# Kernel optimization log

Measured on AMD Instinct MI355X. Metric: run time of the kernel, lower is better.

## Reference

```python
import jax, jax.numpy as jnp
import numpy as np

NUM_STUDENTS = 50000
NUM_KP = 100
KD = 128          # knowledge_dim
HID = 256         # hidden_dim
B = 16384
K = 20            # max_knowledge_points


def setup_inputs() -> dict:
    key = jax.random.key(0)
    ks = jax.random.split(key, 16)
    inp = {
        "student_indices": jax.random.randint(ks[0], (B,), 0, NUM_STUDENTS, dtype=jnp.int32),
        "kp_indices": jax.random.randint(ks[1], (B, K), 0, NUM_KP, dtype=jnp.int32),
        "kp_lengths": jax.random.randint(ks[2], (B,), 0, K + 1, dtype=jnp.int32),
        # learned parameters
        "emb": jax.random.normal(ks[3], (NUM_STUDENTS, NUM_KP, KD), dtype=jnp.float32),
        # attention: Linear(KD,HID) -> tanh -> Linear(HID,1) -> softmax(dim=1)
        "W1": jax.random.normal(ks[4], (KD, HID), dtype=jnp.float32) * 0.05,
        "b1": jnp.zeros((HID,), jnp.float32),
        "w2": jax.random.normal(ks[5], (HID, 1), dtype=jnp.float32) * 0.05,
        "b2": jnp.zeros((1,), jnp.float32),
        # MLP: Linear(KD,HID)-ReLU-Linear(HID,HID//2)-ReLU-Linear(HID//2,1)-Sigmoid
        "M1": jax.random.normal(ks[6], (KD, HID), dtype=jnp.float32) * 0.05,
        "mb1": jnp.zeros((HID,), jnp.float32),
        "M2": jax.random.normal(ks[7], (HID, HID // 2), dtype=jnp.float32) * 0.05,
        "mb2": jnp.zeros((HID // 2,), jnp.float32),
        "M3": jax.random.normal(ks[8], (HID // 2, 1), dtype=jnp.float32) * 0.05,
        "mb3": jnp.zeros((1,), jnp.float32),
    }
    return inp


def reference(student_indices, kp_indices, kp_lengths, emb, W1, b1, w2, b2,
              M1, mb1, M2, mb2, M3, mb3):
    # ragged gather -> padded [B, K, KD]; padded slots are zero (as in the torch loop)
    vecs = emb[student_indices[:, None], kp_indices]            # [B,K,KD]
    mask = (jnp.arange(K)[None, :] < kp_lengths[:, None]).astype(vecs.dtype)  # [B,K]
    vecs = vecs * mask[:, :, None]
    # attention: Linear-Tanh-Linear-Softmax(dim=1), THEN masked (matches original order)
    logits = jnp.tanh(vecs @ W1 + b1) @ w2 + b2                 # [B,K,1]
    att = jax.nn.softmax(logits, axis=1) * mask[:, :, None]     # [B,K,1]
    weighted = jnp.sum(att * vecs, axis=1)                      # [B,KD]
    # MLP (dropout = identity in eval)
    h = jax.nn.relu(weighted @ M1 + mb1)
    h = jax.nn.relu(h @ M2 + mb2)
    scores = jax.nn.sigmoid(h @ M3 + mb3)[:, 0]                 # [B]
    return scores, att[:, :, 0]
```

## Files before the change

### kernel.cpp

```cpp
#include <hip/hip_runtime.h>
#include <hip/hip_bf16.h>

#define K_ 20
#define KD_ 128
#define HID_ 256
#define NKP_ 100

using short8_t = __attribute__((ext_vector_type(8))) short;
using f32x4 = __attribute__((ext_vector_type(4))) float;

__device__ __forceinline__ unsigned short f2bf(float f) {
    union { __hip_bfloat16 h; unsigned short u; } c; c.h = __float2bfloat16(f); return c.u;
}
__device__ __forceinline__ float vexp(float x) { float r; asm("v_exp_f32 %0, %1" : "=v"(r) : "v"(x)); return r; }
__device__ __forceinline__ float vrcp(float x) { float r; asm("v_rcp_f32 %0, %1" : "=v"(r) : "v"(x)); return r; }
__device__ __forceinline__ float bf_lo(unsigned u) { return __uint_as_float(u << 16); }
__device__ __forceinline__ float bf_hi(unsigned u) { return __uint_as_float(u & 0xffff0000u); }

#define CEXP 2.885390081777927f

__global__ __launch_bounds__(256) void prep_frags(
    const float* __restrict__ W1, const float* __restrict__ M1,
    const float* __restrict__ M2, unsigned short* __restrict__ w1f,
    unsigned short* __restrict__ m1f, unsigned short* __restrict__ m2f)
{
    const int b = blockIdx.x;
    const float* src; unsigned short* dst; int nc, smask, nshift, ib;
    if (b < 128)      { src = W1; dst = w1f; nc = 256; smask = 3; nshift = 2; ib = b; }
    else if (b < 256) { src = M1; dst = m1f; nc = 256; smask = 3; nshift = 2; ib = b - 128; }
    else              { src = M2; dst = m2f; nc = 128; smask = 7; nshift = 3; ib = b - 256; }
    const int i = ib * 256 + threadIdx.x;
    const int j = i & 7, l = (i >> 3) & 63, f = i >> 9;
    const int s = f & smask, n = f >> nshift;
    const int k = s * 32 + (l >> 4) * 8 + j;
    const int col = n * 16 + (l & 15);
    dst[i] = f2bf(src[k * nc + col]);
}

__global__ __launch_bounds__(256, 3) void cdm_attn(
    const int* __restrict__ stu_idx, const int* __restrict__ kp_idx,
    const int* __restrict__ kp_len, const float* __restrict__ emb,
    const unsigned short* __restrict__ w1f,
    const float* __restrict__ b1, const float* __restrict__ w2,
    const float* __restrict__ b2,
    float* __restrict__ out_att, unsigned short* __restrict__ wsum_g)
{
    const int tid = threadIdx.x, lane = tid & 63, w = tid >> 6;
    const int base = blockIdx.x * 8;

    __shared__ unsigned short vec_s[8][K_][KD_];
    __shared__ float lp_s[4][2][4][24];
    __shared__ float l0_s[4];
    __shared__ int   len_s[8];

    {
        const int g = lane >> 4, c16 = lane & 15;
        float4 va[10], vb[10];
        int lens[2];
#pragma unroll
        for (int h = 0; h < 2; ++h) {
            const int gs = base + 2 * w + h;
            lens[h] = kp_len[gs];
            const long long eb = (long long)stu_idx[gs] * (NKP_ * KD_);
#pragma unroll
            for (int it = 0; it < 5; ++it) {
                const int q = h * 5 + it;
                va[q] = make_float4(0.f, 0.f, 0.f, 0.f);
                vb[q] = make_float4(0.f, 0.f, 0.f, 0.f);
                const int r = it * 4 + g;
                if (r < lens[h]) {
                    const int kp = kp_idx[gs * K_ + r];
                    const float4* src = (const float4*)(emb + eb + (long long)kp * KD_) + c16 * 2;
                    va[q] = src[0]; vb[q] = src[1];
                }
            }
        }
#pragma unroll
        for (int h = 0; h < 2; ++h) {
            char* sb = (char*)&vec_s[2 * w + h][0][0];
#pragma unroll
            for (int it = 0; it < 5; ++it) {
                const int q = h * 5 + it;
                const int r = it * 4 + g;
                short8_t pk;
                pk[0] = (short)f2bf(va[q].x); pk[1] = (short)f2bf(va[q].y);
                pk[2] = (short)f2bf(va[q].z); pk[3] = (short)f2bf(va[q].w);
                pk[4] = (short)f2bf(vb[q].x); pk[5] = (short)f2bf(vb[q].y);
                pk[6] = (short)f2bf(vb[q].z); pk[7] = (short)f2bf(vb[q].w);
                *(short8_t*)(sb + r * 256 + ((c16 * 16) ^ ((r & 7) << 4))) = pk;
            }
        }
        if (lane == 0) { len_s[2 * w] = lens[0]; len_s[2 * w + 1] = lens[1]; }
    }

    short8_t Bf[4][4];
    {
        const short8_t* bfr = (const short8_t*)w1f;
#pragma unroll
        for (int nn = 0; nn < 4; ++nn)
#pragma unroll
            for (int s = 0; s < 4; ++s)
                Bf[nn][s] = bfr[((w * 4 + nn) * 4 + s) * 64 + lane];
    }
    float b1C[4], w2r[4], n2r[4];
#pragma unroll
    for (int nn = 0; nn < 4; ++nn) {
        const int c = (w * 4 + nn) * 16 + (lane & 15);
        b1C[nn] = b1[c] * CEXP;
        w2r[nn] = w2[c];
        n2r[nn] = -2.f * w2r[nn];
    }
    const float b2v = b2[0];

    {
        float p = 0.f;
#pragma unroll
        for (int nn = 0; nn < 4; ++nn)
            p = fmaf(n2r[nn], vrcp(vexp(b1C[nn]) + 1.f), p + w2r[nn]);
#pragma unroll
        for (int m = 1; m <= 8; m <<= 1) p += __shfl_xor(p, m);
        if (lane == 0) l0_s[w] = p;
    }
    __syncthreads();
    const float logit0 = l0_s[0] + l0_s[1] + l0_s[2] + l0_s[3] + b2v;

#pragma unroll
    for (int p = 0; p < 4; ++p) {
        const int sp = 2 * p;
        const int lA = len_s[sp], lB = len_s[sp + 1];
        const bool need2 = (lA > 16) || (lB > 16);

        short8_t A0[4], A1[4];
        {
            const char* bA = (const char*)&vec_s[sp][0][0];
            const char* bB = (const char*)&vec_s[sp + 1][0][0];
            const int lr = lane & 15;
            const int rowb = lr * 256;
#pragma unroll
            for (int s = 0; s < 4; ++s) {
                const int colA = (s * 64 + (lane >> 4) * 16) ^ ((lr & 7) << 4);
                A0[s] = *(const short8_t*)(bA + rowb + colA);
                A1[s] = *(const short8_t*)(bB + rowb + colA);
            }
        }

        float lp0[4] = {0, 0, 0, 0}, lp1[4] = {0, 0, 0, 0};
#pragma unroll
        for (int nn = 0; nn < 4; ++nn) {
            f32x4 a0 = {0.f, 0.f, 0.f, 0.f}, a1 = {0.f, 0.f, 0.f, 0.f};
#pragma unroll
            for (int s = 0; s < 4; ++s) {
                a0 = __builtin_amdgcn_mfma_f32_16x16x32_bf16(A0[s], Bf[nn][s], a0, 0, 0, 0);
                a1 = __builtin_amdgcn_mfma_f32_16x16x32_bf16(A1[s], Bf[nn][s], a1, 0, 0, 0);
            }
            const float bc = b1C[nn], wv = w2r[nn], n2 = n2r[nn];
#pragma unroll
            for (int i = 0; i < 4; ++i) {
                lp0[i] = fmaf(n2, vrcp(vexp(fmaf(a0[i], CEXP, bc)) + 1.f), lp0[i] + wv);
                lp1[i] = fmaf(n2, vrcp(vexp(fmaf(a1[i], CEXP, bc)) + 1.f), lp1[i] + wv);
            }
        }
#pragma unroll
        for (int i = 0; i < 4; ++i) {
#pragma unroll
            for (int m = 1; m <= 8; m <<= 1) {
                lp0[i] += __shfl_xor(lp0[i], m);
                lp1[i] += __shfl_xor(lp1[i], m);
            }
        }
        if ((lane & 15) == 0) {
            const int g = lane >> 4;
#pragma unroll
            for (int i = 0; i < 4; ++i) {
                lp_s[p][0][w][g * 4 + i] = lp0[i];
                lp_s[p][1][w][g * 4 + i] = lp1[i];
            }
        }

        if (need2) {
            short8_t A2[4];
            const int lr = lane & 15;
            const char* t2b = (const char*)&vec_s[sp + ((lr >> 2) & 1)][0][0] + (16 + (lr & 3)) * 256;
            const bool v2 = lr < 8;
            const short8_t z = {0, 0, 0, 0, 0, 0, 0, 0};
#pragma unroll
            for (int s = 0; s < 4; ++s) {
                const int colT = s * 64 + (lane >> 4) * 16;
                const short8_t t = *(const short8_t*)(t2b + (colT ^ ((lr & 3) << 4)));
                A2[s] = v2 ? t : z;
            }
            float lp2[4] = {0, 0, 0, 0};
#pragma unroll
            for (int nn = 0; nn < 4; ++nn) {
                f32x4 a2 = {0.f, 0.f, 0.f, 0.f};
#pragma unroll
                for (int s = 0; s < 4; ++s)
                    a2 = __builtin_amdgcn_mfma_f32_16x16x32_bf16(A2[s], Bf[nn][s], a2, 0, 0, 0);
                const float bc = b1C[nn], wv = w2r[nn], n2 = n2r[nn];
#pragma unroll
                for (int i = 0; i < 4; ++i)
                    lp2[i] = fmaf(n2, vrcp(vexp(fmaf(a2[i], CEXP, bc)) + 1.f), lp2[i] + wv);
            }
#pragma unroll
            for (int i = 0; i < 4; ++i) {
#pragma unroll
                for (int m = 1; m <= 8; m <<= 1) lp2[i] += __shfl_xor(lp2[i], m);
            }
            if ((lane & 15) == 0 && (lane >> 4) < 2) {
                const int g = lane >> 4;
#pragma unroll
                for (int i = 0; i < 4; ++i) lp_s[p][g][w][16 + i] = lp2[i];
            }
        }
    }
    __syncthreads();

    {
        const int j = lane & 31, hh = lane >> 5;
        const int smp = 2 * w + hh;
        const int gsS = base + smp;
        const int lenS = len_s[smp];
        float logit = -1e30f;
        if (j < K_) {
            logit = (j < lenS)
                ? b2v + lp_s[w][hh][0][j] + lp_s[w][hh][1][j]
                      + lp_s[w][hh][2][j] + lp_s[w][hh][3][j]
                : logit0;
        }
        float mx = logit;
#pragma unroll
        for (int m = 16; m >= 1; m >>= 1) mx = fmaxf(mx, __shfl_xor(mx, m, 32));
        const float e = (j < K_) ? vexp((logit - mx) * 1.44269504f) : 0.f;
        float sm = e;
#pragma unroll
        for (int m = 16; m >= 1; m >>= 1) sm += __shfl_xor(sm, m, 32);
        const float attv = (j < lenS) ? e * vrcp(sm) : 0.f;
        if (j < K_) out_att[gsS * K_ + j] = attv;

        const int d0 = (lane & 31) * 4;
        const char* vb2 = (const char*)&vec_s[smp][0][0];
        const int lm = max(len_s[2 * w], len_s[2 * w + 1]);
        float s0 = 0.f, s1 = 0.f, s2 = 0.f, s3 = 0.f;
        for (int k = 0; k < lm; ++k) {
            const float av = __shfl(attv, k + (lane & 32));
            const uint2 u = *(const uint2*)(vb2 + k * 256 + ((2 * d0) ^ ((k & 7) << 4)));
            s0 = fmaf(av, bf_lo(u.x), s0);
            s1 = fmaf(av, bf_hi(u.x), s1);
            s2 = fmaf(av, bf_lo(u.y), s2);
            s3 = fmaf(av, bf_hi(u.y), s3);
        }
        uint2 pk;
        pk.x = (unsigned)f2bf(s0) | ((unsigned)f2bf(s1) << 16);
        pk.y = (unsigned)f2bf(s2) | ((unsigned)f2bf(s3) << 16);
        *(uint2*)(wsum_g + gsS * KD_ + d0) = pk;
    }
}

__global__ __launch_bounds__(256, 3) void cdm_mlp(
    const unsigned short* __restrict__ wsum_g,
    const unsigned short* __restrict__ m1f, const unsigned short* __restrict__ m2f,
    const float* __restrict__ mb1, const float* __restrict__ mb2,
    const float* __restrict__ M3, const float* __restrict__ mb3,
    float* __restrict__ out_scores)
{
    const int tid = threadIdx.x, lane = tid & 63, w = tid >> 6;
    const int S0 = blockIdx.x * 32;

    __shared__ unsigned short h1_s[32][HID_];
    __shared__ float sc_s[4][32];

    short8_t Aw[2][4];
#pragma unroll
    for (int m = 0; m < 2; ++m)
#pragma unroll
        for (int s = 0; s < 4; ++s)
            Aw[m][s] = *(const short8_t*)(wsum_g + (S0 + m * 16 + (lane & 15)) * KD_
                                          + s * 32 + (lane >> 4) * 8);
    short8_t B1r[4][4];
    {
        const short8_t* bf1 = (const short8_t*)m1f;
#pragma unroll
        for (int nn = 0; nn < 4; ++nn)
#pragma unroll
            for (int s = 0; s < 4; ++s)
                B1r[nn][s] = bf1[((w * 4 + nn) * 4 + s) * 64 + lane];
    }
#pragma unroll
    for (int nn = 0; nn < 4; ++nn) {
        f32x4 c0 = {0.f, 0.f, 0.f, 0.f}, c1 = {0.f, 0.f, 0.f, 0.f};
#pragma unroll
        for (int s = 0; s < 4; ++s) {
            c0 = __builtin_amdgcn_mfma_f32_16x16x32_bf16(Aw[0][s], B1r[nn][s], c0, 0, 0, 0);
            c1 = __builtin_amdgcn_mfma_f32_16x16x32_bf16(Aw[1][s], B1r[nn][s], c1, 0, 0, 0);
        }
        const int col = (w * 4 + nn) * 16 + (lane & 15);
        const float bias = mb1[col];
#pragma unroll
        for (int i = 0; i < 4; ++i) {
            const int r0 = (lane >> 4) * 4 + i;
            const int r1 = 16 + r0;
            *(unsigned short*)((char*)h1_s + r0 * 512 + ((2 * col) ^ ((r0 & 7) << 4)))
                = f2bf(fmaxf(c0[i] + bias, 0.f));
            *(unsigned short*)((char*)h1_s + r1 * 512 + ((2 * col) ^ ((r0 & 7) << 4)))
                = f2bf(fmaxf(c1[i] + bias, 0.f));
        }
    }
    __syncthreads();

    short8_t B2r[2][8];
    {
        const short8_t* bf2 = (const short8_t*)m2f;
#pragma unroll
        for (int nn = 0; nn < 2; ++nn)
#pragma unroll
            for (int s = 0; s < 8; ++s)
                B2r[nn][s] = bf2[((w * 2 + nn) * 8 + s) * 64 + lane];
    }
    f32x4 d00 = {0.f, 0.f, 0.f, 0.f}, d01 = {0.f, 0.f, 0.f, 0.f};
    f32x4 d10 = {0.f, 0.f, 0.f, 0.f}, d11 = {0.f, 0.f, 0.f, 0.f};
    {
        const int lr = lane & 15;
#pragma unroll
        for (int s = 0; s < 8; ++s) {
            const int off = (s * 64 + (lane >> 4) * 16) ^ ((lr & 7) << 4);
            const short8_t Ah0 = *(const short8_t*)((const char*)h1_s + lr * 512 + off);
            const short8_t Ah1 = *(const short8_t*)((const char*)h1_s + (16 + lr) * 512 + off);
            d00 = __builtin_amdgcn_mfma_f32_16x16x32_bf16(Ah0, B2r[0][s], d00, 0, 0, 0);
            d01 = __builtin_amdgcn_mfma_f32_16x16x32_bf16(Ah0, B2r[1][s], d01, 0, 0, 0);
            d10 = __builtin_amdgcn_mfma_f32_16x16x32_bf16(Ah1, B2r[0][s], d10, 0, 0, 0);
            d11 = __builtin_amdgcn_mfma_f32_16x16x32_bf16(Ah1, B2r[1][s], d11, 0, 0, 0);
        }
    }
    float part0[4] = {0, 0, 0, 0}, part1[4] = {0, 0, 0, 0};
#pragma unroll
    for (int nn = 0; nn < 2; ++nn) {
        const int col = (w * 2 + nn) * 16 + (lane & 15);
        const float bb = mb2[col], m3v = M3[col];
        const f32x4 dm0 = nn ? d01 : d00;
        const f32x4 dm1 = nn ? d11 : d10;
#pragma unroll
        for (int i = 0; i < 4; ++i) {
            part0[i] = fmaf(fmaxf(dm0[i] + bb, 0.f), m3v, part0[i]);
            part1[i] = fmaf(fmaxf(dm1[i] + bb, 0.f), m3v, part1[i]);
        }
    }
#pragma unroll
    for (int i = 0; i < 4; ++i) {
#pragma unroll
        for (int m = 1; m <= 8; m <<= 1) {
            part0[i] += __shfl_xor(part0[i], m);
            part1[i] += __shfl_xor(part1[i], m);
        }
    }
    if ((lane & 15) == 0) {
        const int g = lane >> 4;
#pragma unroll
        for (int i = 0; i < 4; ++i) {
            sc_s[w][g * 4 + i] = part0[i];
            sc_s[w][16 + g * 4 + i] = part1[i];
        }
    }
    __syncthreads();
    if (tid < 32) {
        const float sc = sc_s[0][tid] + sc_s[1][tid] + sc_s[2][tid] + sc_s[3][tid] + mb3[0];
        out_scores[S0 + tid] = 1.f / (1.f + __expf(-sc));
    }
}

extern "C" void kernel_launch(void* const* d_in, const int* in_sizes, int n_in,
                              void* d_out, int out_size, void* d_ws, size_t ws_size,
                              hipStream_t stream) {
    const int*   stu = (const int*)d_in[0];
    const int*   kpi = (const int*)d_in[1];
    const int*   kpl = (const int*)d_in[2];
    const float* emb = (const float*)d_in[3];
    const float* W1  = (const float*)d_in[4];
    const float* b1  = (const float*)d_in[5];
    const float* w2  = (const float*)d_in[6];
    const float* b2  = (const float*)d_in[7];
    const float* M1  = (const float*)d_in[8];
    const float* mb1 = (const float*)d_in[9];
    const float* M2  = (const float*)d_in[10];
    const float* mb2 = (const float*)d_in[11];
    const float* M3  = (const float*)d_in[12];
    const float* mb3 = (const float*)d_in[13];
    const int B = in_sizes[0];

    float* out_scores = (float*)d_out;
    float* out_att    = out_scores + B;

    unsigned short* w1f  = (unsigned short*)d_ws;
    unsigned short* m1f  = w1f + 32768;
    unsigned short* m2f  = m1f + 32768;
    unsigned short* wsum = m2f + 32768;

    prep_frags<<<384, 256, 0, stream>>>(W1, M1, M2, w1f, m1f, m2f);
    cdm_attn<<<B / 8, 256, 0, stream>>>(stu, kpi, kpl, emb, w1f, b1, w2, b2,
                                        out_att, wsum);
    cdm_mlp<<<B / 32, 256, 0, stream>>>(wsum, m1f, m2f, mb1, mb2, M3, mb3, out_scores);
}
```

Measured before the change: 78.08 us.

## Double MLP rows per block, hoist index loads, stage attention weights in LDS

The MLP kernel now processes 64 samples per block instead of 32, so the M1/M2 weight fragments loaded into registers are reused over twice as many rows. Launch bounds are relaxed to let it use more registers. In the attention kernel, all kp_idx, stu_idx and length loads are issued before the gather, so the dependent embedding loads no longer wait on index loads one at a time. The weighted-sum loop reads attention weights from a small LDS array instead of using cross-lane shuffles. In exchange, the MLP grid shrinks by half and its occupancy may drop.

```diff
diff --git a/kernel.cpp b/kernel.cpp
--- a/kernel.cpp
+++ b/kernel.cpp
@@ -52,16 +52,24 @@
     __shared__ float lp_s[4][2][4][24];
     __shared__ float l0_s[4];
     __shared__ int   len_s[8];
-
-    {
-        const int g = lane >> 4, c16 = lane & 15;
+    __shared__ float att_s[8][K_];
+
+    const int g = lane >> 4, c16 = lane & 15;
+    int lens[2]; long long eb[2]; int kpr[2][5];
+#pragma unroll
+    for (int h = 0; h < 2; ++h) {
+        const int gs = base + 2 * w + h;
+        lens[h] = kp_len[gs];
+        eb[h] = (long long)stu_idx[gs] * (NKP_ * KD_);
+#pragma unroll
+        for (int it = 0; it < 5; ++it)
+            kpr[h][it] = kp_idx[gs * K_ + it * 4 + g];
+    }
+
+    {
         float4 va[10], vb[10];
-        int lens[2];
 #pragma unroll
         for (int h = 0; h < 2; ++h) {
-            const int gs = base + 2 * w + h;
-            lens[h] = kp_len[gs];
-            const long long eb = (long long)stu_idx[gs] * (NKP_ * KD_);
 #pragma unroll
             for (int it = 0; it < 5; ++it) {
                 const int q = h * 5 + it;
@@ -69,8 +77,7 @@
                 vb[q] = make_float4(0.f, 0.f, 0.f, 0.f);
                 const int r = it * 4 + g;
                 if (r < lens[h]) {
-                    const int kp = kp_idx[gs * K_ + r];
-                    const float4* src = (const float4*)(emb + eb + (long long)kp * KD_) + c16 * 2;
+                    const float4* src = (const float4*)(emb + eb[h] + (long long)kpr[h][it] * KD_) + c16 * 2;
                     va[q] = src[0]; vb[q] = src[1];
                 }
             }
@@ -169,11 +176,11 @@
             }
         }
         if ((lane & 15) == 0) {
-            const int g = lane >> 4;
+            const int gq = lane >> 4;
 #pragma unroll
             for (int i = 0; i < 4; ++i) {
-                lp_s[p][0][w][g * 4 + i] = lp0[i];
-                lp_s[p][1][w][g * 4 + i] = lp1[i];
+                lp_s[p][0][w][gq * 4 + i] = lp0[i];
+                lp_s[p][1][w][gq * 4 + i] = lp1[i];
             }
         }
 
@@ -207,9 +214,9 @@
                 for (int m = 1; m <= 8; m <<= 1) lp2[i] += __shfl_xor(lp2[i], m);
             }
             if ((lane & 15) == 0 && (lane >> 4) < 2) {
-                const int g = lane >> 4;
-#pragma unroll
-                for (int i = 0; i < 4; ++i) lp_s[p][g][w][16 + i] = lp2[i];
+                const int gq = lane >> 4;
+#pragma unroll
+                for (int i = 0; i < 4; ++i) lp_s[p][gq][w][16 + i] = lp2[i];
             }
         }
     }
@@ -235,14 +242,14 @@
 #pragma unroll
         for (int m = 16; m >= 1; m >>= 1) sm += __shfl_xor(sm, m, 32);
         const float attv = (j < lenS) ? e * vrcp(sm) : 0.f;
-        if (j < K_) out_att[gsS * K_ + j] = attv;
+        if (j < K_) { att_s[smp][j] = attv; out_att[gsS * K_ + j] = attv; }
 
         const int d0 = (lane & 31) * 4;
         const char* vb2 = (const char*)&vec_s[smp][0][0];
         const int lm = max(len_s[2 * w], len_s[2 * w + 1]);
         float s0 = 0.f, s1 = 0.f, s2 = 0.f, s3 = 0.f;
         for (int k = 0; k < lm; ++k) {
-            const float av = __shfl(attv, k + (lane & 32));
+            const float av = att_s[smp][k];
             const uint2 u = *(const uint2*)(vb2 + k * 256 + ((2 * d0) ^ ((k & 7) << 4)));
             s0 = fmaf(av, bf_lo(u.x), s0);
             s1 = fmaf(av, bf_hi(u.x), s1);
@@ -256,7 +263,7 @@
     }
 }
 
-__global__ __launch_bounds__(256, 3) void cdm_mlp(
+__global__ __launch_bounds__(256, 2) void cdm_mlp(
     const unsigned short* __restrict__ wsum_g,
     const unsigned short* __restrict__ m1f, const unsigned short* __restrict__ m2f,
     const float* __restrict__ mb1, const float* __restrict__ mb2,
@@ -264,14 +271,14 @@
     float* __restrict__ out_scores)
 {
     const int tid = threadIdx.x, lane = tid & 63, w = tid >> 6;
-    const int S0 = blockIdx.x * 32;
-
-    __shared__ unsigned short h1_s[32][HID_];
-    __shared__ float sc_s[4][32];
-
-    short8_t Aw[2][4];
-#pragma unroll
-    for (int m = 0; m < 2; ++m)
+    const int S0 = blockIdx.x * 64;
+
+    __shared__ unsigned short h1_s[64][HID_];
+    __shared__ float sc_s[4][64];
+
+    short8_t Aw[4][4];
+#pragma unroll
+    for (int m = 0; m < 4; ++m)
 #pragma unroll
         for (int s = 0; s < 4; ++s)
             Aw[m][s] = *(const short8_t*)(wsum_g + (S0 + m * 16 + (lane & 15)) * KD_
@@ -287,23 +294,24 @@
     }
 #pragma unroll
     for (int nn = 0; nn < 4; ++nn) {
-        f32x4 c0 = {0.f, 0.f, 0.f, 0.f}, c1 = {0.f, 0.f, 0.f, 0.f};
-#pragma unroll
-        for (int s = 0; s < 4; ++s) {
-            c0 = __builtin_amdgcn_mfma_f32_16x16x32_bf16(Aw[0][s], B1r[nn][s], c0, 0, 0, 0);
-            c1 = __builtin_amdgcn_mfma_f32_16x16x32_bf16(Aw[1][s], B1r[nn][s], c1, 0, 0, 0);
-        }
+        f32x4 c[4];
+#pragma unroll
+        for (int m = 0; m < 4; ++m) { c[m][0] = 0.f; c[m][1] = 0.f; c[m][2] = 0.f; c[m][3] = 0.f; }
+#pragma unroll
+        for (int s = 0; s < 4; ++s)
+#pragma unroll
+            for (int m = 0; m < 4; ++m)
+                c[m] = __builtin_amdgcn_mfma_f32_16x16x32_bf16(Aw[m][s], B1r[nn][s], c[m], 0, 0, 0);
         const int col = (w * 4 + nn) * 16 + (lane & 15);
         const float bias = mb1[col];
 #pragma unroll
-        for (int i = 0; i < 4; ++i) {
-            const int r0 = (lane >> 4) * 4 + i;
-            const int r1 = 16 + r0;
-            *(unsigned short*)((char*)h1_s + r0 * 512 + ((2 * col) ^ ((r0 & 7) << 4)))
-                = f2bf(fmaxf(c0[i] + bias, 0.f));
-            *(unsigned short*)((char*)h1_s + r1 * 512 + ((2 * col) ^ ((r0 & 7) << 4)))
-                = f2bf(fmaxf(c1[i] + bias, 0.f));
-        }
+        for (int m = 0; m < 4; ++m)
+#pragma unroll
+            for (int i = 0; i < 4; ++i) {
+                const int r0 = m * 16 + (lane >> 4) * 4 + i;
+                *(unsigned short*)((char*)h1_s + r0 * 512 + ((2 * col) ^ ((r0 & 7) << 4)))
+                    = f2bf(fmaxf(c[m][i] + bias, 0.f));
+            }
     }
     __syncthreads();
 
@@ -316,52 +324,44 @@
             for (int s = 0; s < 8; ++s)
                 B2r[nn][s] = bf2[((w * 2 + nn) * 8 + s) * 64 + lane];
     }
-    f32x4 d00 = {0.f, 0.f, 0.f, 0.f}, d01 = {0.f, 0.f, 0.f, 0.f};
-    f32x4 d10 = {0.f, 0.f, 0.f, 0.f}, d11 = {0.f, 0.f, 0.f, 0.f};
+    const int c0 = (w * 2) * 16 + (lane & 15), c1 = c0 + 16;
+    const float mbA = mb2[c0], m3A = M3[c0];
+    const float mbB = mb2[c1], m3B = M3[c1];
+    float part[4][4];
     {
         const int lr = lane & 15;
 #pragma unroll
-        for (int s = 0; s < 8; ++s) {
-            const int off = (s * 64 + (lane >> 4) * 16) ^ ((lr & 7) << 4);
-            const short8_t Ah0 = *(const short8_t*)((const char*)h1_s + lr * 512 + off);
-            const short8_t Ah1 = *(const short8_t*)((const char*)h1_s + (16 + lr) * 512 + off);
-            d00 = __builtin_amdgcn_mfma_f32_16x16x32_bf16(Ah0, B2r[0][s], d00, 0, 0, 0);
-            d01 = __builtin_amdgcn_mfma_f32_16x16x32_bf16(Ah0, B2r[1][s], d01, 0, 0, 0);
-            d10 = __builtin_amdgcn_mfma_f32_16x16x32_bf16(Ah1, B2r[0][s], d10, 0, 0, 0);
-            d11 = __builtin_amdgcn_mfma_f32_16x16x32_bf16(Ah1, B2r[1][s], d11, 0, 0, 0);
-        }
-    }
-    float part0[4] = {0, 0, 0, 0}, part1[4] = {0, 0, 0, 0};
-#pragma unroll
-    for (int nn = 0; nn < 2; ++nn) {
-        const int col = (w * 2 + nn) * 16 + (lane & 15);
-        const float bb = mb2[col], m3v = M3[col];
-        const f32x4 dm0 = nn ? d01 : d00;
-        const f32x4 dm1 = nn ? d11 : d10;
+        for (int m = 0; m < 4; ++m) {
+            f32x4 d0 = {0.f, 0.f, 0.f, 0.f}, d1 = {0.f, 0.f, 0.f, 0.f};
+#pragma unroll
+            for (int s = 0; s < 8; ++s) {
+                const int off = (s * 64 + (lane >> 4) * 16) ^ ((lr & 7) << 4);
+                const short8_t Ah = *(const short8_t*)((const char*)h1_s + (m * 16 + lr) * 512 + off);
+                d0 = __builtin_amdgcn_mfma_f32_16x16x32_bf16(Ah, B2r[0][s], d0, 0, 0, 0);
+                d1 = __builtin_amdgcn_mfma_f32_16x16x32_bf16(Ah, B2r[1][s], d1, 0, 0, 0);
+            }
+#pragma unroll
+            for (int i = 0; i < 4; ++i)
+                part[m][i] = fmaxf(d0[i] + mbA, 0.f) * m3A + fmaxf(d1[i] + mbB, 0.f) * m3B;
+        }
+    }
+#pragma unroll
+    for (int m = 0; m < 4; ++m)
 #pragma unroll
         for (int i = 0; i < 4; ++i) {
-            part0[i] = fmaf(fmaxf(dm0[i] + bb, 0.f), m3v, part0[i]);
-            part1[i] = fmaf(fmaxf(dm1[i] + bb, 0.f), m3v, part1[i]);
-        }
-    }
-#pragma unroll
-    for (int i = 0; i < 4; ++i) {
-#pragma unroll
-        for (int m = 1; m <= 8; m <<= 1) {
-            part0[i] += __shfl_xor(part0[i], m);
-            part1[i] += __shfl_xor(part1[i], m);
-        }
-    }
+#pragma unroll
+            for (int q = 1; q <= 8; q <<= 1) part[m][i] += __shfl_xor(part[m][i], q);
+        }
     if ((lane & 15) == 0) {
-        const int g = lane >> 4;
-#pragma unroll
-        for (int i = 0; i < 4; ++i) {
-            sc_s[w][g * 4 + i] = part0[i];
-            sc_s[w][16 + g * 4 + i] = part1[i];
-        }
+        const int gq = lane >> 4;
+#pragma unroll
+        for (int m = 0; m < 4; ++m)
+#pragma unroll
+            for (int i = 0; i < 4; ++i)
+                sc_s[w][m * 16 + gq * 4 + i] = part[m][i];
     }
     __syncthreads();
-    if (tid < 32) {
+    if (tid < 64) {
         const float sc = sc_s[0][tid] + sc_s[1][tid] + sc_s[2][tid] + sc_s[3][tid] + mb3[0];
         out_scores[S0 + tid] = 1.f / (1.f + __expf(-sc));
     }
@@ -397,5 +397,5 @@
     prep_frags<<<384, 256, 0, stream>>>(W1, M1, M2, w1f, m1f, m2f);
     cdm_attn<<<B / 8, 256, 0, stream>>>(stu, kpi, kpl, emb, w1f, b1, w2, b2,
                                         out_att, wsum);
-    cdm_mlp<<<B / 32, 256, 0, stream>>>(wsum, m1f, m2f, mb1, mb2, M3, mb3, out_scores);
+    cdm_mlp<<<B / 64, 256, 0, stream>>>(wsum, m1f, m2f, mb1, mb2, M3, mb3, out_scores);
 }
```

New measurement: 72.38 us. 7.3% less time.

## Hoist index loads, stage attention weights in LDS, widen MLP blocks to 512 threads

Applied to the files above, without the earlier changes.

The attention kernel now loads all kp indices, lengths and student offsets up front, before the embedding gathers, so the dependent index loads are no longer serialized with the row loads. Attention weights are written to shared memory and read back in the weighted-sum loop in place of per-iteration cross-lane shuffles. The MLP kernel moves to 512 threads (8 waves), so each wave computes half as many output columns with fewer fragment registers, and the final reduction sums 8 partials. This adds LDS traffic and changes occupancy trade-offs.

```diff
diff --git a/kernel.cpp b/kernel.cpp
--- a/kernel.cpp
+++ b/kernel.cpp
@@ -52,16 +52,24 @@
     __shared__ float lp_s[4][2][4][24];
     __shared__ float l0_s[4];
     __shared__ int   len_s[8];
-
-    {
-        const int g = lane >> 4, c16 = lane & 15;
+    __shared__ float att_s[8][K_];
+
+    const int g = lane >> 4, c16 = lane & 15;
+    int lens[2]; long long eb[2]; int kpr[2][5];
+#pragma unroll
+    for (int h = 0; h < 2; ++h) {
+        const int gs = base + 2 * w + h;
+        lens[h] = kp_len[gs];
+        eb[h] = (long long)stu_idx[gs] * (NKP_ * KD_);
+#pragma unroll
+        for (int it = 0; it < 5; ++it)
+            kpr[h][it] = kp_idx[gs * K_ + it * 4 + g];
+    }
+
+    {
         float4 va[10], vb[10];
-        int lens[2];
 #pragma unroll
         for (int h = 0; h < 2; ++h) {
-            const int gs = base + 2 * w + h;
-            lens[h] = kp_len[gs];
-            const long long eb = (long long)stu_idx[gs] * (NKP_ * KD_);
 #pragma unroll
             for (int it = 0; it < 5; ++it) {
                 const int q = h * 5 + it;
@@ -69,8 +77,7 @@
                 vb[q] = make_float4(0.f, 0.f, 0.f, 0.f);
                 const int r = it * 4 + g;
                 if (r < lens[h]) {
-                    const int kp = kp_idx[gs * K_ + r];
-                    const float4* src = (const float4*)(emb + eb + (long long)kp * KD_) + c16 * 2;
+                    const float4* src = (const float4*)(emb + eb[h] + (long long)kpr[h][it] * KD_) + c16 * 2;
                     va[q] = src[0]; vb[q] = src[1];
                 }
             }
@@ -169,11 +176,11 @@
             }
         }
         if ((lane & 15) == 0) {
-            const int g = lane >> 4;
+            const int gq = lane >> 4;
 #pragma unroll
             for (int i = 0; i < 4; ++i) {
-                lp_s[p][0][w][g * 4 + i] = lp0[i];
-                lp_s[p][1][w][g * 4 + i] = lp1[i];
+                lp_s[p][0][w][gq * 4 + i] = lp0[i];
+                lp_s[p][1][w][gq * 4 + i] = lp1[i];
             }
         }
 
@@ -207,9 +214,9 @@
                 for (int m = 1; m <= 8; m <<= 1) lp2[i] += __shfl_xor(lp2[i], m);
             }
             if ((lane & 15) == 0 && (lane >> 4) < 2) {
-                const int g = lane >> 4;
-#pragma unroll
-                for (int i = 0; i < 4; ++i) lp_s[p][g][w][16 + i] = lp2[i];
+                const int gq = lane >> 4;
+#pragma unroll
+                for (int i = 0; i < 4; ++i) lp_s[p][gq][w][16 + i] = lp2[i];
             }
         }
     }
@@ -235,14 +242,14 @@
 #pragma unroll
         for (int m = 16; m >= 1; m >>= 1) sm += __shfl_xor(sm, m, 32);
         const float attv = (j < lenS) ? e * vrcp(sm) : 0.f;
-        if (j < K_) out_att[gsS * K_ + j] = attv;
+        if (j < K_) { att_s[smp][j] = attv; out_att[gsS * K_ + j] = attv; }
 
         const int d0 = (lane & 31) * 4;
         const char* vb2 = (const char*)&vec_s[smp][0][0];
         const int lm = max(len_s[2 * w], len_s[2 * w + 1]);
         float s0 = 0.f, s1 = 0.f, s2 = 0.f, s3 = 0.f;
         for (int k = 0; k < lm; ++k) {
-            const float av = __shfl(attv, k + (lane & 32));
+            const float av = att_s[smp][k];
             const uint2 u = *(const uint2*)(vb2 + k * 256 + ((2 * d0) ^ ((k & 7) << 4)));
             s0 = fmaf(av, bf_lo(u.x), s0);
             s1 = fmaf(av, bf_hi(u.x), s1);
@@ -256,7 +263,7 @@
     }
 }
 
-__global__ __launch_bounds__(256, 3) void cdm_mlp(
+__global__ __launch_bounds__(512) void cdm_mlp(
     const unsigned short* __restrict__ wsum_g,
     const unsigned short* __restrict__ m1f, const unsigned short* __restrict__ m2f,
     const float* __restrict__ mb1, const float* __restrict__ mb2,
@@ -265,39 +272,40 @@
 {
     const int tid = threadIdx.x, lane = tid & 63, w = tid >> 6;
     const int S0 = blockIdx.x * 32;
+    const int lr = lane & 15, g = lane >> 4;
 
     __shared__ unsigned short h1_s[32][HID_];
-    __shared__ float sc_s[4][32];
+    __shared__ float sc_s[8][32];
 
     short8_t Aw[2][4];
 #pragma unroll
     for (int m = 0; m < 2; ++m)
 #pragma unroll
         for (int s = 0; s < 4; ++s)
-            Aw[m][s] = *(const short8_t*)(wsum_g + (S0 + m * 16 + (lane & 15)) * KD_
-                                          + s * 32 + (lane >> 4) * 8);
-    short8_t B1r[4][4];
+            Aw[m][s] = *(const short8_t*)(wsum_g + (S0 + m * 16 + lr) * KD_
+                                          + s * 32 + g * 8);
+    short8_t B1r[2][4];
     {
         const short8_t* bf1 = (const short8_t*)m1f;
 #pragma unroll
-        for (int nn = 0; nn < 4; ++nn)
+        for (int nn = 0; nn < 2; ++nn)
 #pragma unroll
             for (int s = 0; s < 4; ++s)
-                B1r[nn][s] = bf1[((w * 4 + nn) * 4 + s) * 64 + lane];
-    }
-#pragma unroll
-    for (int nn = 0; nn < 4; ++nn) {
+                B1r[nn][s] = bf1[((w * 2 + nn) * 4 + s) * 64 + lane];
+    }
+#pragma unroll
+    for (int nn = 0; nn < 2; ++nn) {
         f32x4 c0 = {0.f, 0.f, 0.f, 0.f}, c1 = {0.f, 0.f, 0.f, 0.f};
 #pragma unroll
         for (int s = 0; s < 4; ++s) {
             c0 = __builtin_amdgcn_mfma_f32_16x16x32_bf16(Aw[0][s], B1r[nn][s], c0, 0, 0, 0);
             c1 = __builtin_amdgcn_mfma_f32_16x16x32_bf16(Aw[1][s], B1r[nn][s], c1, 0, 0, 0);
         }
-        const int col = (w * 4 + nn) * 16 + (lane & 15);
+        const int col = (w * 2 + nn) * 16 + lr;
         const float bias = mb1[col];
 #pragma unroll
         for (int i = 0; i < 4; ++i) {
-            const int r0 = (lane >> 4) * 4 + i;
+            const int r0 = g * 4 + i;
             const int r1 = 16 + r0;
             *(unsigned short*)((char*)h1_s + r0 * 512 + ((2 * col) ^ ((r0 & 7) << 4)))
                 = f2bf(fmaxf(c0[i] + bias, 0.f));
@@ -307,62 +315,51 @@
     }
     __syncthreads();
 
-    short8_t B2r[2][8];
+    short8_t B2r[8];
     {
         const short8_t* bf2 = (const short8_t*)m2f;
 #pragma unroll
-        for (int nn = 0; nn < 2; ++nn)
-#pragma unroll
-            for (int s = 0; s < 8; ++s)
-                B2r[nn][s] = bf2[((w * 2 + nn) * 8 + s) * 64 + lane];
-    }
-    f32x4 d00 = {0.f, 0.f, 0.f, 0.f}, d01 = {0.f, 0.f, 0.f, 0.f};
-    f32x4 d10 = {0.f, 0.f, 0.f, 0.f}, d11 = {0.f, 0.f, 0.f, 0.f};
-    {
-        const int lr = lane & 15;
-#pragma unroll
-        for (int s = 0; s < 8; ++s) {
-            const int off = (s * 64 + (lane >> 4) * 16) ^ ((lr & 7) << 4);
-            const short8_t Ah0 = *(const short8_t*)((const char*)h1_s + lr * 512 + off);
-            const short8_t Ah1 = *(const short8_t*)((const char*)h1_s + (16 + lr) * 512 + off);
-            d00 = __builtin_amdgcn_mfma_f32_16x16x32_bf16(Ah0, B2r[0][s], d00, 0, 0, 0);
-            d01 = __builtin_amdgcn_mfma_f32_16x16x32_bf16(Ah0, B2r[1][s], d01, 0, 0, 0);
-            d10 = __builtin_amdgcn_mfma_f32_16x16x32_bf16(Ah1, B2r[0][s], d10, 0, 0, 0);
-            d11 = __builtin_amdgcn_mfma_f32_16x16x32_bf16(Ah1, B2r[1][s], d11, 0, 0, 0);
-        }
-    }
-    float part0[4] = {0, 0, 0, 0}, part1[4] = {0, 0, 0, 0};
-#pragma unroll
-    for (int nn = 0; nn < 2; ++nn) {
-        const int col = (w * 2 + nn) * 16 + (lane & 15);
+        for (int s = 0; s < 8; ++s)
+            B2r[s] = bf2[(w * 8 + s) * 64 + lane];
+    }
+    f32x4 d0 = {0.f, 0.f, 0.f, 0.f}, d1 = {0.f, 0.f, 0.f, 0.f};
+#pragma unroll
+    for (int s = 0; s < 8; ++s) {
+        const int off = (s * 64 + g * 16) ^ ((lr & 7) << 4);
+        const short8_t Ah0 = *(const short8_t*)((const char*)h1_s + lr * 512 + off);
+        const short8_t Ah1 = *(const short8_t*)((const char*)h1_s + (16 + lr) * 512 + off);
+        d0 = __builtin_amdgcn_mfma_f32_16x16x32_bf16(Ah0, B2r[s], d0, 0, 0, 0);
+        d1 = __builtin_amdgcn_mfma_f32_16x16x32_bf16(Ah1, B2r[s], d1, 0, 0, 0);
+    }
+    {
+        const int col = w * 16 + lr;
         const float bb = mb2[col], m3v = M3[col];
-        const f32x4 dm0 = nn ? d01 : d00;
-        const f32x4 dm1 = nn ? d11 : d10;
+        float part0[4], part1[4];
 #pragma unroll
         for (int i = 0; i < 4; ++i) {
-            part0[i] = fmaf(fmaxf(dm0[i] + bb, 0.f), m3v, part0[i]);
-            part1[i] = fmaf(fmaxf(dm1[i] + bb, 0.f), m3v, part1[i]);
-        }
-    }
-#pragma unroll
-    for (int i = 0; i < 4; ++i) {
-#pragma unroll
-        for (int m = 1; m <= 8; m <<= 1) {
-            part0[i] += __shfl_xor(part0[i], m);
-            part1[i] += __shfl_xor(part1[i], m);
-        }
-    }
-    if ((lane & 15) == 0) {
-        const int g = lane >> 4;
+            part0[i] = fmaxf(d0[i] + bb, 0.f) * m3v;
+            part1[i] = fmaxf(d1[i] + bb, 0.f) * m3v;
+        }
 #pragma unroll
         for (int i = 0; i < 4; ++i) {
-            sc_s[w][g * 4 + i] = part0[i];
-            sc_s[w][16 + g * 4 + i] = part1[i];
+#pragma unroll
+            for (int q = 1; q <= 8; q <<= 1) {
+                part0[i] += __shfl_xor(part0[i], q);
+                part1[i] += __shfl_xor(part1[i], q);
+            }
+        }
+        if (lr == 0) {
+#pragma unroll
+            for (int i = 0; i < 4; ++i) {
+                sc_s[w][g * 4 + i]      = part0[i];
+                sc_s[w][16 + g * 4 + i] = part1[i];
+            }
         }
     }
     __syncthreads();
     if (tid < 32) {
-        const float sc = sc_s[0][tid] + sc_s[1][tid] + sc_s[2][tid] + sc_s[3][tid] + mb3[0];
+        const float sc = sc_s[0][tid] + sc_s[1][tid] + sc_s[2][tid] + sc_s[3][tid]
+                       + sc_s[4][tid] + sc_s[5][tid] + sc_s[6][tid] + sc_s[7][tid] + mb3[0];
         out_scores[S0 + tid] = 1.f / (1.f + __expf(-sc));
     }
 }
@@ -397,5 +394,5 @@
     prep_frags<<<384, 256, 0, stream>>>(W1, M1, M2, w1f, m1f, m2f);
     cdm_attn<<<B / 8, 256, 0, stream>>>(stu, kpi, kpl, emb, w1f, b1, w2, b2,
                                         out_att, wsum);
-    cdm_mlp<<<B / 32, 256, 0, stream>>>(wsum, m1f, m2f, mb1, mb2, M3, mb3, out_scores);
-}
+    cdm_mlp<<<B / 32, 512, 0, stream>>>(wsum, m1f, m2f, mb1, mb2, M3, mb3, out_scores);
+}
```

New measurement: 71.84 us (median of 2 runs). 8.0% less time.
